# Optimization experiments

Measured on AMD Instinct MI355X. Metric: run time of the kernel, lower is better.

The kernel has to match this reference:

```python
import jax, jax.numpy as jnp
import numpy as np

O, P, G, N, H, D = 3, 128, 64, 20000, 512, 128
TEMPERATURE = 0.1
EPS = 1e-12


def setup_inputs() -> dict:
    key = jax.random.key(0)
    k0, k1, k2, k3 = jax.random.split(key, 4)
    emb = jax.random.normal(k0, (O, N, H), dtype=jnp.float32)
    idx = jax.random.randint(k1, (O, P, G), 0, N)
    W1 = jax.random.normal(k2, (O, H, H), dtype=jnp.float32) * 0.02
    b1 = jnp.zeros((O, H), dtype=jnp.float32)
    W2 = jax.random.normal(k3, (O, H, D), dtype=jnp.float32) * 0.02
    b2 = jnp.zeros((O, D), dtype=jnp.float32)
    return {"emb": emb, "W1": W1, "b1": b1, "W2": W2, "b2": b2, "idx": idx}


def reference(emb, W1, b1, W2, b2, idx):
    # Per-omics pathway prototypes: gather gene rows then mean-pool.  [O,P,H]
    protos = jax.vmap(lambda e, i: jnp.mean(e[i], axis=1))(emb, idx)
    # Per-omics projection head: Linear -> ReLU -> (Dropout=identity in eval) -> Linear
    h = jax.nn.relu(jnp.einsum('oph,ohk->opk', protos, W1) + b1[:, None, :])
    z = jnp.einsum('opk,okd->opd', h, W2) + b2[:, None, :]          # [O,P,D]
    # Original loops p outer, ntype inner -> order (pathway, omics)
    z = jnp.transpose(z, (1, 0, 2)).reshape(P * O, D)                # [M,D], M=P*O
    z = z / (jnp.linalg.norm(z, axis=-1, keepdims=True) + EPS)       # l2 normalize
    y = jnp.repeat(jnp.arange(P), O)                                 # pathway labels [M]

    sim = (z @ z.T) / TEMPERATURE                                    # [M,M]
    M = sim.shape[0]
    eye = jnp.eye(M, dtype=bool)
    sim = jnp.where(eye, -jnp.inf, sim)
    pos_mask = (y[None, :] == y[:, None]) & ~eye
    exp_sim = jnp.exp(sim)                                           # exp(-inf)=0 on diagonal
    denom = exp_sim.sum(axis=1) + EPS
    pos_sum = jnp.sum(exp_sim * pos_mask.astype(exp_sim.dtype), axis=1) + EPS
    # every anchor has O-1 positives here, so all anchors are valid
    loss = -jnp.log(pos_sum / denom)
    return loss.mean()
```

## Files before the change

### kernel.cpp

```cpp
#include <hip/hip_runtime.h>
#include <math.h>

#define O_ 3
#define P_ 128
#define G_ 64
#define N_ 20000
#define H_ 512
#define D_ 128
#define M_ (O_*P_)

static constexpr float TEMP_INV = 10.0f;
static constexpr float EPS_ = 1e-12f;

__global__ __launch_bounds__(512) void k_protos(const float* __restrict__ emb,
                                                const int* __restrict__ idx,
                                                float* __restrict__ protos) {
    const int b = blockIdx.x;
    const int o = b >> 7;
    const int t = threadIdx.x;
    const int q = t >> 7, c4 = t & 127;

    __shared__ int sIdx[G_];
    __shared__ float4 sRed[4][128];

    if (t < G_) sIdx[t] = idx[b * G_ + t];
    __syncthreads();

    const float* base = emb + (size_t)o * N_ * H_ + (size_t)c4 * 4;
    float4 acc = make_float4(0.f, 0.f, 0.f, 0.f);
    #pragma unroll
    for (int g = 0; g < 16; ++g) {
        const float4 v = *(const float4*)(base + (size_t)((unsigned)sIdx[q * 16 + g]) * H_);
        acc.x += v.x; acc.y += v.y; acc.z += v.z; acc.w += v.w;
    }
    sRed[q][c4] = acc;
    __syncthreads();

    if (q == 0) {
        const float4 a0 = sRed[0][c4], a1 = sRed[1][c4];
        const float4 a2 = sRed[2][c4], a3 = sRed[3][c4];
        const float s = 1.0f / (float)G_;
        float4 r;
        r.x = (a0.x + a1.x + a2.x + a3.x) * s;
        r.y = (a0.y + a1.y + a2.y + a3.y) * s;
        r.z = (a0.z + a1.z + a2.z + a3.z) * s;
        r.w = (a0.w + a1.w + a2.w + a3.w) * s;
        ((float4*)(protos + (size_t)b * H_))[c4] = r;
    }
}

__global__ __launch_bounds__(512) void k_gemm1(const float* __restrict__ protos,
                                               const float* __restrict__ W1,
                                               const float* __restrict__ b1,
                                               float* __restrict__ hbuf) {
    const int b = blockIdx.x;
    const int o = b >> 7;
    const int t = threadIdx.x;
    const int ks = t >> 7, kq = t & 127;

    __shared__ float sP[H_];
    __shared__ float4 sPart[4][128];

    sP[t] = protos[(size_t)b * H_ + t];
    __syncthreads();

    const float4* w1 = (const float4*)(W1 + (size_t)o * H_ * H_) + kq;
    float4 acc = make_float4(0.f, 0.f, 0.f, 0.f);
    const int h0 = ks * 128;
    #pragma unroll 8
    for (int h = 0; h < 128; ++h) {
        const float a = sP[h0 + h];
        const float4 w = w1[(size_t)(h0 + h) * 128];
        acc.x = fmaf(a, w.x, acc.x);
        acc.y = fmaf(a, w.y, acc.y);
        acc.z = fmaf(a, w.z, acc.z);
        acc.w = fmaf(a, w.w, acc.w);
    }
    sPart[ks][kq] = acc;
    __syncthreads();

    if (ks == 0) {
        const float4 r0 = sPart[0][kq], r1 = sPart[1][kq];
        const float4 r2 = sPart[2][kq], r3 = sPart[3][kq];
        const float4 bb = ((const float4*)(b1 + (size_t)o * H_))[kq];
        float4 r;
        r.x = fmaxf(r0.x + r1.x + r2.x + r3.x + bb.x, 0.f);
        r.y = fmaxf(r0.y + r1.y + r2.y + r3.y + bb.y, 0.f);
        r.z = fmaxf(r0.z + r1.z + r2.z + r3.z + bb.z, 0.f);
        r.w = fmaxf(r0.w + r1.w + r2.w + r3.w + bb.w, 0.f);
        ((float4*)(hbuf + (size_t)b * H_))[kq] = r;
    }
}

__global__ __launch_bounds__(512) void k_gemm2_norm(const float* __restrict__ hbuf,
                                                    const float* __restrict__ W2,
                                                    const float* __restrict__ b2,
                                                    float* __restrict__ z) {
    const int b = blockIdx.x;
    const int o = b >> 7, p = b & 127;
    const int t = threadIdx.x;
    const int ks = t >> 5, dq = t & 31;

    __shared__ float sH[H_];
    __shared__ float4 sPart[16][32];
    __shared__ float sZ[D_];
    __shared__ float sNr[2];

    sH[t] = hbuf[(size_t)b * H_ + t];
    __syncthreads();

    const float4* w2 = (const float4*)(W2 + (size_t)o * H_ * D_) + dq;
    float4 acc = make_float4(0.f, 0.f, 0.f, 0.f);
    const int h0 = ks * 32;
    #pragma unroll 8
    for (int h = 0; h < 32; ++h) {
        const float a = sH[h0 + h];
        const float4 w = w2[(size_t)(h0 + h) * 32];
        acc.x = fmaf(a, w.x, acc.x);
        acc.y = fmaf(a, w.y, acc.y);
        acc.z = fmaf(a, w.z, acc.z);
        acc.w = fmaf(a, w.w, acc.w);
    }
    sPart[ks][dq] = acc;
    __syncthreads();

    if (t < 32) {
        float4 s = make_float4(0.f, 0.f, 0.f, 0.f);
        #pragma unroll
        for (int j = 0; j < 16; ++j) {
            const float4 v = sPart[j][t];
            s.x += v.x; s.y += v.y; s.z += v.z; s.w += v.w;
        }
        const float4 bb = ((const float4*)(b2 + (size_t)o * D_))[t];
        s.x += bb.x; s.y += bb.y; s.z += bb.z; s.w += bb.w;
        ((float4*)sZ)[t] = s;
    }
    __syncthreads();

    if (t < D_) {
        const float v = sZ[t];
        float s = v * v;
        #pragma unroll
        for (int off = 32; off > 0; off >>= 1) s += __shfl_down(s, off, 64);
        if ((t & 63) == 0) sNr[t >> 6] = s;
    }
    __syncthreads();
    if (t < D_) {
        const float inv = 1.0f / (sqrtf(sNr[0] + sNr[1]) + EPS_);
        z[(size_t)(p * O_ + o) * D_ + t] = sZ[t] * inv;
    }
}

__global__ __launch_bounds__(256) void k_loss(const float* __restrict__ z,
                                              float* __restrict__ out) {
    const int i = blockIdx.x;
    const int t = threadIdx.x;
    __shared__ float zi[D_];
    if (t < D_) zi[t] = z[(size_t)i * D_ + t];
    __syncthreads();
    const int pi = i / 3;
    float denom = 0.f, pos = 0.f;
    const float4* zi4 = (const float4*)zi;
    #pragma unroll
    for (int jj = 0; jj < 2; ++jj) {
        const int j = t + jj * 256;
        if (j < M_) {
            const float4* zj = (const float4*)(z + (size_t)j * D_);
            float dot = 0.f;
            #pragma unroll 8
            for (int q = 0; q < D_ / 4; ++q) {
                const float4 a = zi4[q];
                const float4 bb = zj[q];
                dot = fmaf(a.x, bb.x, fmaf(a.y, bb.y, fmaf(a.z, bb.z, fmaf(a.w, bb.w, dot))));
            }
            if (j != i) {
                const float e = __expf(dot * TEMP_INV);
                denom += e;
                if (j / 3 == pi) pos += e;
            }
        }
    }
    #pragma unroll
    for (int off = 32; off > 0; off >>= 1) {
        denom += __shfl_down(denom, off, 64);
        pos   += __shfl_down(pos,   off, 64);
    }
    __shared__ float rd[4], rp[4];
    const int lane = t & 63, wid = t >> 6;
    if (lane == 0) { rd[wid] = denom; rp[wid] = pos; }
    __syncthreads();
    if (t == 0) {
        const float dn = rd[0] + rd[1] + rd[2] + rd[3] + EPS_;
        const float ps = rp[0] + rp[1] + rp[2] + rp[3] + EPS_;
        const float loss_i = logf(dn) - logf(ps);
        atomicAdd(out, loss_i * (1.0f / (float)M_));
    }
}

extern "C" void kernel_launch(void* const* d_in, const int* in_sizes, int n_in,
                              void* d_out, int out_size, void* d_ws, size_t ws_size,
                              hipStream_t stream) {
    const float* emb = (const float*)d_in[0];
    const float* W1  = (const float*)d_in[1];
    const float* b1  = (const float*)d_in[2];
    const float* W2  = (const float*)d_in[3];
    const float* b2  = (const float*)d_in[4];
    const int*   idx = (const int*)d_in[5];

    float* ws     = (float*)d_ws;
    float* protos = ws;
    float* hbuf   = ws + 196608;
    float* zbuf   = ws + 393216;

    hipMemsetAsync(d_out, 0, sizeof(float), stream);

    k_protos    <<<dim3(M_), dim3(512), 0, stream>>>(emb, idx, protos);
    k_gemm1     <<<dim3(M_), dim3(512), 0, stream>>>(protos, W1, b1, hbuf);
    k_gemm2_norm<<<dim3(M_), dim3(512), 0, stream>>>(hbuf, W2, b2, zbuf);
    k_loss      <<<dim3(M_), dim3(256), 0, stream>>>(zbuf, (float*)d_out);
}
```

Measured before the change: 223.3 us.

## Tile gemm1 over 8 pathways by 64 output columns to reuse W1 loads

```diff
diff --git a/kernel.cpp b/kernel.cpp
--- a/kernel.cpp
+++ b/kernel.cpp
@@ -49,46 +49,58 @@
     }
 }
 
+#define PRSTR 516
 __global__ __launch_bounds__(512) void k_gemm1(const float* __restrict__ protos,
                                                const float* __restrict__ W1,
                                                const float* __restrict__ b1,
                                                float* __restrict__ hbuf) {
-    const int b = blockIdx.x;
-    const int o = b >> 7;
-    const int t = threadIdx.x;
-    const int ks = t >> 7, kq = t & 127;
-
-    __shared__ float sP[H_];
-    __shared__ float4 sPart[4][128];
-
-    sP[t] = protos[(size_t)b * H_ + t];
-    __syncthreads();
-
-    const float4* w1 = (const float4*)(W1 + (size_t)o * H_ * H_) + kq;
+    const int blk = blockIdx.x;
+    const int o = blk >> 7;
+    const int rem = blk & 127;
+    const int pg = rem >> 3, ks = rem & 7;
+    const int p0 = pg * 8, k0 = ks * 64;
+    const int t = threadIdx.x;
+    const int hs = t >> 7, r = (t >> 4) & 7, q4 = t & 15;
+
+    __shared__ float sPr[8 * PRSTR];
+    __shared__ float4 sPart[4][8][16];
+
+    {
+        const float4* src = (const float4*)(protos + (size_t)(o * P_ + p0) * H_);
+        #pragma unroll
+        for (int i = 0; i < 2; ++i) {
+            const int fidx = i * 512 + t;
+            const int rr = fidx >> 7, c4 = fidx & 127;
+            ((float4*)sPr)[rr * (PRSTR / 4) + c4] = src[rr * 128 + c4];
+        }
+    }
+    __syncthreads();
+
+    const float4* w1 = (const float4*)(W1 + (size_t)o * H_ * H_) + (k0 >> 2) + q4;
+    const float* pr = sPr + r * PRSTR + hs * 128;
     float4 acc = make_float4(0.f, 0.f, 0.f, 0.f);
-    const int h0 = ks * 128;
     #pragma unroll 8
     for (int h = 0; h < 128; ++h) {
-        const float a = sP[h0 + h];
-        const float4 w = w1[(size_t)(h0 + h) * 128];
+        const float a = pr[h];
+        const float4 w = w1[(size_t)(hs * 128 + h) * 128];
         acc.x = fmaf(a, w.x, acc.x);
         acc.y = fmaf(a, w.y, acc.y);
         acc.z = fmaf(a, w.z, acc.z);
         acc.w = fmaf(a, w.w, acc.w);
     }
-    sPart[ks][kq] = acc;
-    __syncthreads();
-
-    if (ks == 0) {
-        const float4 r0 = sPart[0][kq], r1 = sPart[1][kq];
-        const float4 r2 = sPart[2][kq], r3 = sPart[3][kq];
-        const float4 bb = ((const float4*)(b1 + (size_t)o * H_))[kq];
-        float4 r;
-        r.x = fmaxf(r0.x + r1.x + r2.x + r3.x + bb.x, 0.f);
-        r.y = fmaxf(r0.y + r1.y + r2.y + r3.y + bb.y, 0.f);
-        r.z = fmaxf(r0.z + r1.z + r2.z + r3.z + bb.z, 0.f);
-        r.w = fmaxf(r0.w + r1.w + r2.w + r3.w + bb.w, 0.f);
-        ((float4*)(hbuf + (size_t)b * H_))[kq] = r;
+    sPart[hs][r][q4] = acc;
+    __syncthreads();
+
+    if (hs == 0) {
+        const float4 r0 = sPart[0][r][q4], r1 = sPart[1][r][q4];
+        const float4 r2 = sPart[2][r][q4], r3 = sPart[3][r][q4];
+        const float4 bb = ((const float4*)(b1 + (size_t)o * H_ + k0))[q4];
+        float4 out;
+        out.x = fmaxf(r0.x + r1.x + r2.x + r3.x + bb.x, 0.f);
+        out.y = fmaxf(r0.y + r1.y + r2.y + r3.y + bb.y, 0.f);
+        out.z = fmaxf(r0.z + r1.z + r2.z + r3.z + bb.z, 0.f);
+        out.w = fmaxf(r0.w + r1.w + r2.w + r3.w + bb.w, 0.f);
+        ((float4*)(hbuf + (size_t)(o * P_ + p0 + r) * H_ + k0))[q4] = out;
     }
 }
 
```

Result: no change. 219.7 us (-1.6%).

## Fuse gather-mean, both MLP layers and normalization into one kernel

Applied to the files above, without the earlier changes.

```diff
diff --git a/kernel.cpp b/kernel.cpp
--- a/kernel.cpp
+++ b/kernel.cpp
@@ -12,142 +12,129 @@
 static constexpr float TEMP_INV = 10.0f;
 static constexpr float EPS_ = 1e-12f;
 
-__global__ __launch_bounds__(512) void k_protos(const float* __restrict__ emb,
-                                                const int* __restrict__ idx,
-                                                float* __restrict__ protos) {
-    const int b = blockIdx.x;
-    const int o = b >> 7;
-    const int t = threadIdx.x;
-    const int q = t >> 7, c4 = t & 127;
-
-    __shared__ int sIdx[G_];
-    __shared__ float4 sRed[4][128];
-
-    if (t < G_) sIdx[t] = idx[b * G_ + t];
-    __syncthreads();
-
-    const float* base = emb + (size_t)o * N_ * H_ + (size_t)c4 * 4;
-    float4 acc = make_float4(0.f, 0.f, 0.f, 0.f);
-    #pragma unroll
-    for (int g = 0; g < 16; ++g) {
-        const float4 v = *(const float4*)(base + (size_t)((unsigned)sIdx[q * 16 + g]) * H_);
-        acc.x += v.x; acc.y += v.y; acc.z += v.z; acc.w += v.w;
-    }
-    sRed[q][c4] = acc;
-    __syncthreads();
-
-    if (q == 0) {
-        const float4 a0 = sRed[0][c4], a1 = sRed[1][c4];
-        const float4 a2 = sRed[2][c4], a3 = sRed[3][c4];
-        const float s = 1.0f / (float)G_;
-        float4 r;
-        r.x = (a0.x + a1.x + a2.x + a3.x) * s;
-        r.y = (a0.y + a1.y + a2.y + a3.y) * s;
-        r.z = (a0.z + a1.z + a2.z + a3.z) * s;
-        r.w = (a0.w + a1.w + a2.w + a3.w) * s;
-        ((float4*)(protos + (size_t)b * H_))[c4] = r;
-    }
-}
-
-__global__ __launch_bounds__(512) void k_gemm1(const float* __restrict__ protos,
+__global__ __launch_bounds__(512) void k_fused(const float* __restrict__ emb,
+                                               const int* __restrict__ idx,
                                                const float* __restrict__ W1,
                                                const float* __restrict__ b1,
-                                               float* __restrict__ hbuf) {
-    const int b = blockIdx.x;
-    const int o = b >> 7;
-    const int t = threadIdx.x;
-    const int ks = t >> 7, kq = t & 127;
-
-    __shared__ float sP[H_];
-    __shared__ float4 sPart[4][128];
-
-    sP[t] = protos[(size_t)b * H_ + t];
-    __syncthreads();
-
-    const float4* w1 = (const float4*)(W1 + (size_t)o * H_ * H_) + kq;
-    float4 acc = make_float4(0.f, 0.f, 0.f, 0.f);
-    const int h0 = ks * 128;
-    #pragma unroll 8
-    for (int h = 0; h < 128; ++h) {
-        const float a = sP[h0 + h];
-        const float4 w = w1[(size_t)(h0 + h) * 128];
-        acc.x = fmaf(a, w.x, acc.x);
-        acc.y = fmaf(a, w.y, acc.y);
-        acc.z = fmaf(a, w.z, acc.z);
-        acc.w = fmaf(a, w.w, acc.w);
-    }
-    sPart[ks][kq] = acc;
-    __syncthreads();
-
-    if (ks == 0) {
-        const float4 r0 = sPart[0][kq], r1 = sPart[1][kq];
-        const float4 r2 = sPart[2][kq], r3 = sPart[3][kq];
-        const float4 bb = ((const float4*)(b1 + (size_t)o * H_))[kq];
-        float4 r;
-        r.x = fmaxf(r0.x + r1.x + r2.x + r3.x + bb.x, 0.f);
-        r.y = fmaxf(r0.y + r1.y + r2.y + r3.y + bb.y, 0.f);
-        r.z = fmaxf(r0.z + r1.z + r2.z + r3.z + bb.z, 0.f);
-        r.w = fmaxf(r0.w + r1.w + r2.w + r3.w + bb.w, 0.f);
-        ((float4*)(hbuf + (size_t)b * H_))[kq] = r;
-    }
-}
-
-__global__ __launch_bounds__(512) void k_gemm2_norm(const float* __restrict__ hbuf,
-                                                    const float* __restrict__ W2,
-                                                    const float* __restrict__ b2,
-                                                    float* __restrict__ z) {
+                                               const float* __restrict__ W2,
+                                               const float* __restrict__ b2,
+                                               float* __restrict__ z,
+                                               float* __restrict__ out) {
     const int b = blockIdx.x;
     const int o = b >> 7, p = b & 127;
     const int t = threadIdx.x;
-    const int ks = t >> 5, dq = t & 31;
-
-    __shared__ float sH[H_];
-    __shared__ float4 sPart[16][32];
-    __shared__ float sZ[D_];
-    __shared__ float sNr[2];
-
-    sH[t] = hbuf[(size_t)b * H_ + t];
-    __syncthreads();
-
-    const float4* w2 = (const float4*)(W2 + (size_t)o * H_ * D_) + dq;
-    float4 acc = make_float4(0.f, 0.f, 0.f, 0.f);
-    const int h0 = ks * 32;
-    #pragma unroll 8
-    for (int h = 0; h < 32; ++h) {
-        const float a = sH[h0 + h];
-        const float4 w = w2[(size_t)(h0 + h) * 32];
-        acc.x = fmaf(a, w.x, acc.x);
-        acc.y = fmaf(a, w.y, acc.y);
-        acc.z = fmaf(a, w.z, acc.z);
-        acc.w = fmaf(a, w.w, acc.w);
-    }
-    sPart[ks][dq] = acc;
-    __syncthreads();
-
-    if (t < 32) {
-        float4 s = make_float4(0.f, 0.f, 0.f, 0.f);
+
+    __shared__ int    sIdx[G_];
+    __shared__ float  sP[H_];
+    __shared__ float  sH[H_];
+    __shared__ float4 sPart[512];
+    __shared__ float  sZ[D_];
+    __shared__ float  sNr[2];
+
+    if (b == 0 && t == 0) *out = 0.f;
+
+    {
+        const int q = t >> 7, c4 = t & 127;
+        if (t < G_) sIdx[t] = idx[b * G_ + t];
+        __syncthreads();
+
+        const float* base = emb + (size_t)o * N_ * H_ + (size_t)c4 * 4;
+        float4 acc = make_float4(0.f, 0.f, 0.f, 0.f);
         #pragma unroll
-        for (int j = 0; j < 16; ++j) {
-            const float4 v = sPart[j][t];
-            s.x += v.x; s.y += v.y; s.z += v.z; s.w += v.w;
-        }
-        const float4 bb = ((const float4*)(b2 + (size_t)o * D_))[t];
-        s.x += bb.x; s.y += bb.y; s.z += bb.z; s.w += bb.w;
-        ((float4*)sZ)[t] = s;
-    }
-    __syncthreads();
-
-    if (t < D_) {
-        const float v = sZ[t];
-        float s = v * v;
-        #pragma unroll
-        for (int off = 32; off > 0; off >>= 1) s += __shfl_down(s, off, 64);
-        if ((t & 63) == 0) sNr[t >> 6] = s;
-    }
-    __syncthreads();
-    if (t < D_) {
-        const float inv = 1.0f / (sqrtf(sNr[0] + sNr[1]) + EPS_);
-        z[(size_t)(p * O_ + o) * D_ + t] = sZ[t] * inv;
+        for (int g = 0; g < 16; ++g) {
+            const float4 v = *(const float4*)(base + (size_t)((unsigned)sIdx[q * 16 + g]) * H_);
+            acc.x += v.x; acc.y += v.y; acc.z += v.z; acc.w += v.w;
+        }
+        sPart[q * 128 + c4] = acc;
+        __syncthreads();
+
+        if (q == 0) {
+            const float4 a0 = sPart[0 * 128 + c4], a1 = sPart[1 * 128 + c4];
+            const float4 a2 = sPart[2 * 128 + c4], a3 = sPart[3 * 128 + c4];
+            const float s = 1.0f / (float)G_;
+            float4 r;
+            r.x = (a0.x + a1.x + a2.x + a3.x) * s;
+            r.y = (a0.y + a1.y + a2.y + a3.y) * s;
+            r.z = (a0.z + a1.z + a2.z + a3.z) * s;
+            r.w = (a0.w + a1.w + a2.w + a3.w) * s;
+            ((float4*)sP)[c4] = r;
+        }
+    }
+    __syncthreads();
+
+    {
+        const int ks = t >> 7, kq = t & 127;
+        const float4* w1 = (const float4*)(W1 + (size_t)o * H_ * H_) + kq;
+        float4 acc = make_float4(0.f, 0.f, 0.f, 0.f);
+        const int h0 = ks * 128;
+        #pragma unroll 8
+        for (int h = 0; h < 128; ++h) {
+            const float a = sP[h0 + h];
+            const float4 w = w1[(size_t)(h0 + h) * 128];
+            acc.x = fmaf(a, w.x, acc.x);
+            acc.y = fmaf(a, w.y, acc.y);
+            acc.z = fmaf(a, w.z, acc.z);
+            acc.w = fmaf(a, w.w, acc.w);
+        }
+        sPart[ks * 128 + kq] = acc;
+        __syncthreads();
+
+        if (ks == 0) {
+            const float4 r0 = sPart[0 * 128 + kq], r1 = sPart[1 * 128 + kq];
+            const float4 r2 = sPart[2 * 128 + kq], r3 = sPart[3 * 128 + kq];
+            const float4 bb = ((const float4*)(b1 + (size_t)o * H_))[kq];
+            float4 r;
+            r.x = fmaxf(r0.x + r1.x + r2.x + r3.x + bb.x, 0.f);
+            r.y = fmaxf(r0.y + r1.y + r2.y + r3.y + bb.y, 0.f);
+            r.z = fmaxf(r0.z + r1.z + r2.z + r3.z + bb.z, 0.f);
+            r.w = fmaxf(r0.w + r1.w + r2.w + r3.w + bb.w, 0.f);
+            ((float4*)sH)[kq] = r;
+        }
+    }
+    __syncthreads();
+
+    {
+        const int ks16 = t >> 5, dq = t & 31;
+        const float4* w2 = (const float4*)(W2 + (size_t)o * H_ * D_) + dq;
+        float4 acc = make_float4(0.f, 0.f, 0.f, 0.f);
+        const int h0 = ks16 * 32;
+        #pragma unroll 8
+        for (int h = 0; h < 32; ++h) {
+            const float a = sH[h0 + h];
+            const float4 w = w2[(size_t)(h0 + h) * 32];
+            acc.x = fmaf(a, w.x, acc.x);
+            acc.y = fmaf(a, w.y, acc.y);
+            acc.z = fmaf(a, w.z, acc.z);
+            acc.w = fmaf(a, w.w, acc.w);
+        }
+        sPart[ks16 * 32 + dq] = acc;
+        __syncthreads();
+
+        if (t < 32) {
+            float4 s = make_float4(0.f, 0.f, 0.f, 0.f);
+            #pragma unroll
+            for (int j = 0; j < 16; ++j) {
+                const float4 v = sPart[j * 32 + t];
+                s.x += v.x; s.y += v.y; s.z += v.z; s.w += v.w;
+            }
+            const float4 bb = ((const float4*)(b2 + (size_t)o * D_))[t];
+            s.x += bb.x; s.y += bb.y; s.z += bb.z; s.w += bb.w;
+            ((float4*)sZ)[t] = s;
+        }
+        __syncthreads();
+
+        if (t < D_) {
+            const float v = sZ[t];
+            float s = v * v;
+            #pragma unroll
+            for (int off = 32; off > 0; off >>= 1) s += __shfl_down(s, off, 64);
+            if ((t & 63) == 0) sNr[t >> 6] = s;
+        }
+        __syncthreads();
+        if (t < D_) {
+            const float inv = 1.0f / (sqrtf(sNr[0] + sNr[1]) + EPS_);
+            z[(size_t)(p * O_ + o) * D_ + t] = sZ[t] * inv;
+        }
     }
 }
 
@@ -207,15 +194,9 @@
     const float* b2  = (const float*)d_in[4];
     const int*   idx = (const int*)d_in[5];
 
-    float* ws     = (float*)d_ws;
-    float* protos = ws;
-    float* hbuf   = ws + 196608;
-    float* zbuf   = ws + 393216;
-
-    hipMemsetAsync(d_out, 0, sizeof(float), stream);
-
-    k_protos    <<<dim3(M_), dim3(512), 0, stream>>>(emb, idx, protos);
-    k_gemm1     <<<dim3(M_), dim3(512), 0, stream>>>(protos, W1, b1, hbuf);
-    k_gemm2_norm<<<dim3(M_), dim3(512), 0, stream>>>(hbuf, W2, b2, zbuf);
-    k_loss      <<<dim3(M_), dim3(256), 0, stream>>>(zbuf, (float*)d_out);
+    float* zbuf = (float*)d_ws;
+
+    k_fused<<<dim3(M_), dim3(512), 0, stream>>>(emb, idx, W1, b1, W2, b2,
+                                                zbuf, (float*)d_out);
+    k_loss <<<dim3(M_), dim3(256), 0, stream>>>(zbuf, (float*)d_out);
 }
```

Measured after the change: 213.0 us. 1.05x faster.
